# Kernel optimization log

Hardware: AMD Instinct MI355X
Metric: run time of the kernel (lower is better)

## Reference

```python
import jax, jax.numpy as jnp
import numpy as np

B, S, D, H, F, R = 4, 128, 512, 8, 2048, 8
DH = D // H
THRESH = 0.1  # hardcoded in the torch module


def _ln(x, g, b):
    m = x.mean(-1, keepdims=True)
    v = ((x - m) ** 2).mean(-1, keepdims=True)
    return (x - m) * jax.lax.rsqrt(v + 1e-5) * g + b


def setup_inputs() -> dict:
    key = jax.random.key(0)
    ks = jax.random.split(key, 12)
    w = lambda k, shape, std: jax.random.normal(k, shape, jnp.float32) * std
    s = 1.0 / np.sqrt(D)
    qk_std = 2.0 / np.sqrt(D)  # peaky attention so adjacency threshold fires
    return {
        "x": jax.random.normal(ks[0], (B, S, D), jnp.float32),
        "ln1_g": jnp.ones(D, jnp.float32), "ln1_b": jnp.zeros(D, jnp.float32),
        "wq": w(ks[1], (D, D), qk_std), "bq": jnp.zeros(D, jnp.float32),
        "wk": w(ks[2], (D, D), qk_std), "bk": jnp.zeros(D, jnp.float32),
        "wv": w(ks[3], (D, D), s), "bv": jnp.zeros(D, jnp.float32),
        "wo": w(ks[4], (D, D), s), "bo": jnp.zeros(D, jnp.float32),
        "w1": w(ks[5], (D, F), s), "b1": jnp.zeros(F, jnp.float32),
        "w2": w(ks[6], (F, D), 1.0 / np.sqrt(F)), "b2": jnp.zeros(D, jnp.float32),
        "rc_w1": w(ks[7], (2 * D, D), 1.0 / np.sqrt(2 * D)), "rc_b1": jnp.zeros(D, jnp.float32),
        "rc_w2": w(ks[8], (D, R), s), "rc_b2": jnp.zeros(R, jnp.float32),
        "kg_w": w(ks[9], (R, D, D), s),
        "s2n_w": w(ks[10], (D, D), s), "s2n_b": jnp.zeros(D, jnp.float32),
        "ln2_g": jnp.ones(D, jnp.float32), "ln2_b": jnp.zeros(D, jnp.float32),
    }


def reference(x, ln1_g, ln1_b, wq, bq, wk, bk, wv, bv, wo, bo,
              w1, b1, w2, b2, rc_w1, rc_b1, rc_w2, rc_b2,
              kg_w, s2n_w, s2n_b, ln2_g, ln2_b):
    # pre-norm attention
    xn = _ln(x, ln1_g, ln1_b)
    q = (xn @ wq + bq).reshape(B, S, H, DH)
    k = (xn @ wk + bk).reshape(B, S, H, DH)
    v = (xn @ wv + bv).reshape(B, S, H, DH)
    scores = jnp.einsum('bihd,bjhd->bhij', q, k) / np.sqrt(DH)
    attn = jax.nn.softmax(scores, axis=-1)                  # [B,H,S,S]
    ctx = jnp.einsum('bhij,bjhd->bihd', attn, v).reshape(B, S, D)
    attn_out = ctx @ wo + bo
    # FFN -> neural_understanding (no residual, as in source)
    nu = jax.nn.relu(attn_out @ w1 + b1) @ w2 + b2          # [B,S,D]
    # dynamic edge extraction, expressed as a dense mask (jit-safe)
    am = attn.mean(axis=1)                                  # [B,S,S]
    adj = (am > THRESH) & (~jnp.eye(S, dtype=bool))         # u != v
    # relation classifier on every (u,v) pair; mask selects real edges
    a_part = nu @ rc_w1[:D]                                 # concept1 half
    b_part = nu @ rc_w1[D:]                                 # concept2 half
    h = jax.nn.relu(a_part[:, :, None, :] + b_part[:, None, :, :] + rc_b1)  # [B,S,S,D]
    logits = h @ rc_w2 + rc_b2                              # [B,S,S,R]
    pred = jnp.argmax(logits, axis=-1)
    valid = adj & (pred != 0)                               # relation 0 == NONE
    oh = jax.nn.one_hot(pred, R, dtype=nu.dtype) * valid[..., None].astype(nu.dtype)
    # RGCN-style knowledge graph conv: message u -> v with per-relation weight
    transformed = jnp.einsum('bud,rde->bure', nu, kg_w)     # [B,S,R,D]
    agg = jnp.einsum('buvr,bure->bve', oh, transformed)     # [B,S,D]
    reasoned = nu + agg
    neural_result = reasoned @ s2n_w + s2n_b
    out = _ln(x + neural_result, ln2_g, ln2_b)
    return out
```

## Files before the change

### kernel.cpp

```cpp
#include <hip/hip_runtime.h>
#include <hip/hip_bf16.h>

#define B_ 4
#define S_ 128
#define D_ 512
#define H_ 8
#define DH_ 64
#define F_ 2048
#define R_ 8
#define BS_ (B_ * S_)
#define BSD_ (BS_ * D_)
#define E_ 262144

typedef __attribute__((ext_vector_type(8))) short short8;
typedef __attribute__((ext_vector_type(4))) float f32x4;
typedef __attribute__((ext_vector_type(4))) unsigned short ushort4v;

__device__ __forceinline__ void split2(float a, unsigned short& h, unsigned short& l) {
    unsigned u = __float_as_uint(a);
    unsigned hr = (u + 0x7FFFu + ((u >> 16) & 1u)) >> 16;
    h = (unsigned short)hr;
    float lo = a - __uint_as_float(hr << 16);
    unsigned u2 = __float_as_uint(lo);
    l = (unsigned short)((u2 + 0x7FFFu + ((u2 >> 16) & 1u)) >> 16);
}

struct TDesc { const float* s; unsigned short* h; unsigned short* l; int K; int N; int off; };
struct TPack { TDesc d[10]; };

__global__ void prep_kernel(TPack p, int nt, const float* __restrict__ x,
                            const float* __restrict__ g, const float* __restrict__ be,
                            unsigned short* __restrict__ xh, unsigned short* __restrict__ xl,
                            int* __restrict__ ecount) {
    __shared__ float tr[32][33];
    __shared__ float red[256];
    int bid = blockIdx.x;
    if (bid == 0 && threadIdx.x == 0) *ecount = 0;
    if (bid < nt) {
        int wi = 0;
#pragma unroll
        for (int i = 1; i < 10; ++i) if (bid >= p.d[i].off) wi = i;
        const TDesc dd = p.d[wi];
        int t = bid - dd.off;
        int ntk = dd.K / 32;
        int tk = t % ntk, tn = t / ntk;
        int k0 = tk * 32, n0 = tn * 32;
        int col = threadIdx.x & 31, rg = threadIdx.x >> 5;
#pragma unroll
        for (int i = 0; i < 4; ++i) {
            int row = rg * 4 + i;
            tr[row][col] = dd.s[(size_t)(k0 + row) * dd.N + n0 + col];
        }
        __syncthreads();
#pragma unroll
        for (int i = 0; i < 4; ++i) {
            int n = n0 + rg * 4 + i;
            int k = k0 + col;
            unsigned short h, l;
            split2(tr[col][rg * 4 + i], h, l);
            dd.h[(size_t)n * dd.K + k] = h;
            dd.l[(size_t)n * dd.K + k] = l;
        }
    } else {
        int row = bid - nt;
        int t = threadIdx.x;
        const float* xr = x + (size_t)row * D_;
        float v0 = xr[t], v1 = xr[t + 256];
        red[t] = v0 + v1;
        __syncthreads();
        for (int off = 128; off > 0; off >>= 1) { if (t < off) red[t] += red[t + off]; __syncthreads(); }
        float mean = red[0] * (1.0f / D_);
        __syncthreads();
        float d0 = v0 - mean, d1 = v1 - mean;
        red[t] = d0 * d0 + d1 * d1;
        __syncthreads();
        for (int off = 128; off > 0; off >>= 1) { if (t < off) red[t] += red[t + off]; __syncthreads(); }
        float rs = rsqrtf(red[0] * (1.0f / D_) + 1e-5f);
        float o0 = d0 * rs * g[t] + be[t];
        float o1 = d1 * rs * g[t + 256] + be[t + 256];
        unsigned short h, l;
        split2(o0, h, l); xh[(size_t)row * D_ + t] = h;       xl[(size_t)row * D_ + t] = l;
        split2(o1, h, l); xh[(size_t)row * D_ + t + 256] = h; xl[(size_t)row * D_ + t + 256] = l;
    }
}

struct GemmLds {
    unsigned short A[2][2][64][32];
    unsigned short B[2][2][64][32];
};

__device__ __forceinline__ void gload16(const unsigned short* g, unsigned short* l) {
    __builtin_amdgcn_global_load_lds(
        (const __attribute__((address_space(1))) void*)g,
        (__attribute__((address_space(3))) void*)l, 16, 0, 0);
}

__device__ __forceinline__ void mgemm_core(const unsigned short* __restrict__ Ath,
                                           const unsigned short* __restrict__ Atl,
                                           const unsigned short* __restrict__ Bth,
                                           const unsigned short* __restrict__ Btl,
                                           int K, int rowBase, int colBase,
                                           int kStart, int nsteps,
                                           f32x4 acc[2][2], GemmLds* L) {
    int tid = threadIdx.x;
    int w = tid >> 6, lane = tid & 63;
    int lm = lane & 15, quad = lane >> 4;
    int wm = (w & 1) * 32, wn = (w >> 1) * 32;
    int rS = tid >> 2;
    int cSrc = ((tid & 3) ^ (rS & 3)) * 8;
    int wb = w * 512;
    int qs = (quad ^ (lm & 3)) * 8;
    size_t aoff = (size_t)(rowBase + rS) * K + kStart + cSrc;
    size_t boff = (size_t)(colBase + rS) * K + kStart + cSrc;
    gload16(&Ath[aoff], &L->A[0][0][0][0] + wb);
    gload16(&Atl[aoff], &L->A[0][1][0][0] + wb);
    gload16(&Bth[boff], &L->B[0][0][0][0] + wb);
    gload16(&Btl[boff], &L->B[0][1][0][0] + wb);
    __syncthreads();
    for (int s = 0; s < nsteps; ++s) {
        int p = s & 1;
        if (s + 1 < nsteps) {
            int pn = p ^ 1;
            size_t ao = aoff + (size_t)(s + 1) * 32;
            size_t bo = boff + (size_t)(s + 1) * 32;
            gload16(&Ath[ao], &L->A[pn][0][0][0] + wb);
            gload16(&Atl[ao], &L->A[pn][1][0][0] + wb);
            gload16(&Bth[bo], &L->B[pn][0][0][0] + wb);
            gload16(&Btl[bo], &L->B[pn][1][0][0] + wb);
        }
        short8 ah[2], al[2], bh[2], bl[2];
#pragma unroll
        for (int t = 0; t < 2; ++t) {
            ah[t] = *(const short8*)&L->A[p][0][wm + t * 16 + lm][qs];
            al[t] = *(const short8*)&L->A[p][1][wm + t * 16 + lm][qs];
            bh[t] = *(const short8*)&L->B[p][0][wn + t * 16 + lm][qs];
            bl[t] = *(const short8*)&L->B[p][1][wn + t * 16 + lm][qs];
        }
#pragma unroll
        for (int tm = 0; tm < 2; ++tm)
#pragma unroll
            for (int tn = 0; tn < 2; ++tn) {
                acc[tm][tn] = __builtin_amdgcn_mfma_f32_16x16x32_bf16(ah[tm], bh[tn], acc[tm][tn], 0, 0, 0);
                acc[tm][tn] = __builtin_amdgcn_mfma_f32_16x16x32_bf16(ah[tm], bl[tn], acc[tm][tn], 0, 0, 0);
                acc[tm][tn] = __builtin_amdgcn_mfma_f32_16x16x32_bf16(al[tm], bh[tn], acc[tm][tn], 0, 0, 0);
            }
        __syncthreads();
    }
}

__global__ __launch_bounds__(256) void mgemm_kernel(const unsigned short* __restrict__ Ath,
                                                    const unsigned short* __restrict__ Atl,
                                                    const unsigned short* __restrict__ Bth,
                                                    const unsigned short* __restrict__ Btl,
                                                    const float* __restrict__ bias,
                                                    float* __restrict__ Cf,
                                                    unsigned short* __restrict__ Ch,
                                                    unsigned short* __restrict__ Cl,
                                                    int N, int K, int relu) {
    __shared__ GemmLds L;
    int tid = threadIdx.x;
    int w = tid >> 6, lane = tid & 63;
    int lm = lane & 15, quad = lane >> 4;
    int wm = (w & 1) * 32, wn = (w >> 1) * 32;
    int rowBase = blockIdx.y * 64, colBase = blockIdx.x * 64;
    f32x4 acc[2][2] = {};
    mgemm_core(Ath, Atl, Bth, Btl, K, rowBase, colBase, 0, K / 32, acc, &L);
#pragma unroll
    for (int tm = 0; tm < 2; ++tm)
#pragma unroll
        for (int tn = 0; tn < 2; ++tn) {
            int col = colBase + wn + tn * 16 + lm;
            float bi = bias ? bias[col] : 0.f;
#pragma unroll
            for (int r = 0; r < 4; ++r) {
                int row = rowBase + wm + tm * 16 + quad * 4 + r;
                float v = acc[tm][tn][r] + bi;
                if (relu) v = fmaxf(v, 0.f);
                size_t o = (size_t)row * N + col;
                if (Cf) Cf[o] = v;
                if (Ch) {
                    unsigned short sh, sl;
                    split2(v, sh, sl);
                    Ch[o] = sh; Cl[o] = sl;
                }
            }
        }
}

__global__ __launch_bounds__(256) void mgemm_zw_kernel(const unsigned short* __restrict__ Ath,
                                                       const unsigned short* __restrict__ Atl,
                                                       const unsigned short* __restrict__ Bth,
                                                       const unsigned short* __restrict__ Btl,
                                                       const float* __restrict__ b0,
                                                       const float* __restrict__ b1,
                                                       const float* __restrict__ b2,
                                                       float* __restrict__ Cbase,
                                                       int M, int N, int K) {
    __shared__ GemmLds L;
    int z = blockIdx.z;
    const unsigned short* bth = Bth + (size_t)z * K * N;
    const unsigned short* btl = Btl + (size_t)z * K * N;
    const float* bias = (z == 0) ? b0 : (z == 1) ? b1 : b2;
    float* C = Cbase + (size_t)z * M * N;
    int tid = threadIdx.x;
    int w = tid >> 6, lane = tid & 63;
    int lm = lane & 15, quad = lane >> 4;
    int wm = (w & 1) * 32, wn = (w >> 1) * 32;
    int rowBase = blockIdx.y * 64, colBase = blockIdx.x * 64;
    f32x4 acc[2][2] = {};
    mgemm_core(Ath, Atl, bth, btl, K, rowBase, colBase, 0, K / 32, acc, &L);
#pragma unroll
    for (int tm = 0; tm < 2; ++tm)
#pragma unroll
        for (int tn = 0; tn < 2; ++tn) {
            int col = colBase + wn + tn * 16 + lm;
            float bi = bias ? bias[col] : 0.f;
#pragma unroll
            for (int r = 0; r < 4; ++r) {
                int row = rowBase + wm + tm * 16 + quad * 4 + r;
                C[(size_t)row * N + col] = acc[tm][tn][r] + bi;
            }
        }
}

__global__ __launch_bounds__(256) void mgemm_part_kernel(const unsigned short* __restrict__ Ath,
                                                         const unsigned short* __restrict__ Atl,
                                                         const unsigned short* __restrict__ Bth,
                                                         const unsigned short* __restrict__ Btl,
                                                         float* __restrict__ Cbase,
                                                         int M, int N, int K) {
    __shared__ GemmLds L;
    int ks = gridDim.z, z = blockIdx.z;
    int kLen = K / ks, kStart = z * kLen;
    float* C = Cbase + (size_t)z * M * N;
    int tid = threadIdx.x;
    int w = tid >> 6, lane = tid & 63;
    int lm = lane & 15, quad = lane >> 4;
    int wm = (w & 1) * 32, wn = (w >> 1) * 32;
    int rowBase = blockIdx.y * 64, colBase = blockIdx.x * 64;
    f32x4 acc[2][2] = {};
    mgemm_core(Ath, Atl, Bth, Btl, K, rowBase, colBase, kStart, kLen / 32, acc, &L);
#pragma unroll
    for (int tm = 0; tm < 2; ++tm)
#pragma unroll
        for (int tn = 0; tn < 2; ++tn) {
            int col = colBase + wn + tn * 16 + lm;
#pragma unroll
            for (int r = 0; r < 4; ++r) {
                int row = rowBase + wm + tm * 16 + quad * 4 + r;
                C[(size_t)row * N + col] = acc[tm][tn][r];
            }
        }
}

__global__ void reduce4_kernel(const float* __restrict__ part, const float* __restrict__ b2,
                               float* __restrict__ nu,
                               unsigned short* __restrict__ nh, unsigned short* __restrict__ nl) {
    int base = blockIdx.x * 1024 + threadIdx.x * 4;
    f32x4 s = *(const f32x4*)&b2[base & (D_ - 1)];
#pragma unroll
    for (int z = 0; z < 4; ++z) s += *(const f32x4*)&part[(size_t)z * BSD_ + base];
    *(f32x4*)&nu[base] = s;
    ushort4v hv, lv;
#pragma unroll
    for (int i = 0; i < 4; ++i) { unsigned short h, l; split2(s[i], h, l); hv[i] = h; lv[i] = l; }
    *(ushort4v*)&nh[base] = hv;
    *(ushort4v*)&nl[base] = lv;
}

__global__ void reduce8_kernel(const float* __restrict__ part, const float* __restrict__ nu,
                               unsigned short* __restrict__ rh, unsigned short* __restrict__ rl) {
    int base = blockIdx.x * 1024 + threadIdx.x * 4;
    f32x4 s = *(const f32x4*)&nu[base];
#pragma unroll
    for (int z = 0; z < 8; ++z) s += *(const f32x4*)&part[(size_t)z * BSD_ + base];
    ushort4v hv, lv;
#pragma unroll
    for (int i = 0; i < 4; ++i) { unsigned short h, l; split2(s[i], h, l); hv[i] = h; lv[i] = l; }
    *(ushort4v*)&rh[base] = hv;
    *(ushort4v*)&rl[base] = lv;
}

__global__ __launch_bounds__(512) void attn_fused_kernel(const float* __restrict__ q,
                                                         const float* __restrict__ k,
                                                         const float* __restrict__ v,
                                                         unsigned short* __restrict__ ch,
                                                         unsigned short* __restrict__ cl,
                                                         int* __restrict__ ecount,
                                                         int* __restrict__ elist,
                                                         int* __restrict__ rel) {
    __shared__ float qsm[H_][DH_];
    __shared__ float psm[H_][S_];
    int h = threadIdx.x >> 6, lane = threadIdx.x & 63;
    int blk = blockIdx.x;
    int i = blk & (S_ - 1);
    int b = blk >> 7;
    const float* qrow = q + (size_t)(b * S_ + i) * D_ + h * DH_;
    qsm[h][lane] = qrow[lane];
    __syncthreads();
    float s0 = 0.f, s1 = 0.f;
    const float* k0p = k + (size_t)(b * S_ + lane) * D_ + h * DH_;
    const float* k1p = k0p + (size_t)64 * D_;
#pragma unroll 8
    for (int d = 0; d < DH_; ++d) {
        float qd = qsm[h][d];
        s0 += qd * k0p[d];
        s1 += qd * k1p[d];
    }
    s0 *= 0.125f; s1 *= 0.125f;
    float m = fmaxf(s0, s1);
#pragma unroll
    for (int off = 32; off > 0; off >>= 1) m = fmaxf(m, __shfl_xor(m, off));
    float e0 = __expf(s0 - m), e1 = __expf(s1 - m);
    float sum = e0 + e1;
#pragma unroll
    for (int off = 32; off > 0; off >>= 1) sum += __shfl_xor(sum, off);
    float inv = 1.f / sum;
    psm[h][lane] = e0 * inv;
    psm[h][lane + 64] = e1 * inv;
    __syncthreads();
    if (threadIdx.x < S_) {
        int j = threadIdx.x;
        rel[(size_t)blk * S_ + j] = 0;
        float s = 0.f;
#pragma unroll
        for (int hh = 0; hh < H_; ++hh) s += psm[hh][j];
        s *= (1.0f / H_);
        if (s > 0.1f && i != j) {
            int p = atomicAdd(ecount, 1);
            elist[p] = blk * S_ + j;
        }
    }
    const float* vbase = v + (size_t)b * S_ * D_ + h * DH_ + lane;
    float acc = 0.f;
    for (int j = 0; j < S_; ++j) acc += psm[h][j] * vbase[(size_t)j * D_];
    unsigned short sh, sl;
    split2(acc, sh, sl);
    size_t o = (size_t)(b * S_ + i) * D_ + h * DH_ + lane;
    ch[o] = sh; cl[o] = sl;
}

__global__ __launch_bounds__(256) void edge_kernel(const float* __restrict__ a_part,
                                                   const float* __restrict__ b_part,
                                                   const float* __restrict__ rc_b1,
                                                   const float* __restrict__ rc_w2,
                                                   const float* __restrict__ rc_b2,
                                                   const int* __restrict__ elist,
                                                   const int* __restrict__ ecount,
                                                   int* __restrict__ rel) {
    int w = threadIdx.x >> 6, lane = threadIdx.x & 63;
    int n = *ecount;
    for (int e = blockIdx.x * 4 + w; e < n; e += gridDim.x * 4) {
        int idx = elist[e];
        int vv = idx & (S_ - 1);
        int bu = idx >> 7;
        int u = bu & (S_ - 1);
        int b = bu >> 7;
        const float* ap = a_part + (size_t)(b * S_ + u) * D_;
        const float* bp = b_part + (size_t)(b * S_ + vv) * D_;
        float lp[R_];
#pragma unroll
        for (int r = 0; r < R_; ++r) lp[r] = 0.f;
#pragma unroll
        for (int jj = 0; jj < D_ / 64; ++jj) {
            int d = lane + jj * 64;
            float hv = fmaxf(ap[d] + bp[d] + rc_b1[d], 0.f);
#pragma unroll
            for (int r = 0; r < R_; ++r) lp[r] += hv * rc_w2[d * R_ + r];
        }
#pragma unroll
        for (int r = 0; r < R_; ++r) {
#pragma unroll
            for (int off = 32; off > 0; off >>= 1) lp[r] += __shfl_down(lp[r], off);
        }
        if (lane == 0) {
            float best = lp[0] + rc_b2[0];
            int bi = 0;
#pragma unroll
            for (int r = 1; r < R_; ++r) {
                float L = lp[r] + rc_b2[r];
                if (L > best) { best = L; bi = r; }
            }
            rel[idx] = bi;
        }
    }
}

__global__ __launch_bounds__(128) void mbuild_kernel(const float* __restrict__ nu,
                                                     const int* __restrict__ rel,
                                                     unsigned short* __restrict__ Mh,
                                                     unsigned short* __restrict__ Ml) {
    __shared__ float acc[R_ * D_];
    __shared__ int rl[S_];
    int blk = blockIdx.x;
    int vv = blk & (S_ - 1);
    int b = blk >> 7;
    int t = threadIdx.x;
    for (int i = t; i < R_ * D_; i += 128) acc[i] = 0.f;
    rl[t] = rel[((size_t)b * S_ + t) * S_ + vv];
    __syncthreads();
    for (int u = 0; u < S_; ++u) {
        int r = rl[u];
        if (r > 0) {
            const float* nurow = nu + (size_t)(b * S_ + u) * D_;
            float* arow = acc + r * D_;
#pragma unroll
            for (int jj = 0; jj < D_ / 128; ++jj) arow[t + jj * 128] += nurow[t + jj * 128];
        }
    }
    __syncthreads();
    unsigned short* Hrow = Mh + (size_t)blk * (R_ * D_);
    unsigned short* Lrow = Ml + (size_t)blk * (R_ * D_);
    for (int i = t; i < R_ * D_; i += 128) {
        unsigned short sh, sl;
        split2(acc[i], sh, sl);
        Hrow[i] = sh; Lrow[i] = sl;
    }
}

__global__ void ln2_kernel(const float* __restrict__ x, const float* __restrict__ y,
                           const float* __restrict__ g, const float* __restrict__ be,
                           float* __restrict__ out) {
    int row = blockIdx.x;
    int t = threadIdx.x;
    __shared__ float red[256];
    float v0 = x[row * D_ + t]       + y[row * D_ + t];
    float v1 = x[row * D_ + t + 256] + y[row * D_ + t + 256];
    red[t] = v0 + v1;
    __syncthreads();
    for (int off = 128; off > 0; off >>= 1) {
        if (t < off) red[t] += red[t + off];
        __syncthreads();
    }
    float mean = red[0] * (1.0f / D_);
    __syncthreads();
    float d0 = v0 - mean, d1 = v1 - mean;
    red[t] = d0 * d0 + d1 * d1;
    __syncthreads();
    for (int off = 128; off > 0; off >>= 1) {
        if (t < off) red[t] += red[t + off];
        __syncthreads();
    }
    float rs = rsqrtf(red[0] * (1.0f / D_) + 1e-5f);
    out[row * D_ + t]       = d0 * rs * g[t]       + be[t];
    out[row * D_ + t + 256] = d1 * rs * g[t + 256] + be[t + 256];
}

extern "C" void kernel_launch(void* const* d_in, const int* in_sizes, int n_in,
                              void* d_out, int out_size, void* d_ws, size_t ws_size,
                              hipStream_t stream) {
    const float* x     = (const float*)d_in[0];
    const float* ln1_g = (const float*)d_in[1];
    const float* ln1_b = (const float*)d_in[2];
    const float* wq    = (const float*)d_in[3];
    const float* bq    = (const float*)d_in[4];
    const float* wk    = (const float*)d_in[5];
    const float* bk    = (const float*)d_in[6];
    const float* wv    = (const float*)d_in[7];
    const float* bv    = (const float*)d_in[8];
    const float* wo    = (const float*)d_in[9];
    const float* bo    = (const float*)d_in[10];
    const float* w1    = (const float*)d_in[11];
    const float* b1    = (const float*)d_in[12];
    const float* w2    = (const float*)d_in[13];
    const float* b2    = (const float*)d_in[14];
    const float* rc_w1 = (const float*)d_in[15];
    const float* rc_b1 = (const float*)d_in[16];
    const float* rc_w2 = (const float*)d_in[17];
    const float* rc_b2 = (const float*)d_in[18];
    const float* kg_w  = (const float*)d_in[19];
    const float* s2n_w = (const float*)d_in[20];
    const float* s2n_b = (const float*)d_in[21];
    const float* ln2_g = (const float*)d_in[22];
    const float* ln2_b = (const float*)d_in[23];
    float* out = (float*)d_out;

    const int BS  = BS_;
    const int BSD = BSD_;

    unsigned short* wt = (unsigned short*)d_ws;
    unsigned short* qkv_h = wt;
    unsigned short* qkv_l = wt + 3 * E_;
    unsigned short* wo_h  = wt + 6 * E_;
    unsigned short* wo_l  = wt + 7 * E_;
    unsigned short* w1_h  = wt + 8 * E_;
    unsigned short* w1_l  = wt + 12 * E_;
    unsigned short* w2_h  = wt + 16 * E_;
    unsigned short* w2_l  = wt + 20 * E_;
    unsigned short* rc_h  = wt + 24 * E_;
    unsigned short* rc_l  = wt + 26 * E_;
    unsigned short* kg_h  = wt + 28 * E_;
    unsigned short* kg_l  = wt + 36 * E_;
    unsigned short* s2_h  = wt + 44 * E_;
    unsigned short* s2_l  = wt + 45 * E_;

    unsigned short* xn_h  = wt + 46 * E_;
    unsigned short* xn_l  = xn_h + BSD;
    unsigned short* ctx_h = xn_l + BSD;
    unsigned short* ctx_l = ctx_h + BSD;
    unsigned short* ao_h  = ctx_l + BSD;
    unsigned short* ao_l  = ao_h + BSD;
    unsigned short* hid_h = ao_l + BSD;
    unsigned short* hid_l = hid_h + (size_t)BS * F_;
    unsigned short* nu_h  = hid_l + (size_t)BS * F_;
    unsigned short* nu_l  = nu_h + BSD;
    unsigned short* mb_h  = nu_l + BSD;
    unsigned short* mb_l  = mb_h + (size_t)BS * R_ * D_;
    unsigned short* rs_h  = mb_l + (size_t)BS * R_ * D_;
    unsigned short* rs_l  = rs_h + BSD;

    float* fbase  = (float*)(rs_l + BSD);
    float* q      = fbase;
    float* v_     = q + 2 * BSD;
    float* apart  = q + 3 * BSD;
    float* nu     = apart + 2 * BSD;
    float* y      = nu + BSD;
    float* part4  = y + BSD;
    float* part8  = part4 + 4 * BSD;

    int* rel    = (int*)(part8 + 8 * BSD);
    int* ecount = rel + B_ * S_ * S_;
    int* elist  = ecount + 64;

    TPack tp;
    int off = 0;
    auto setd = [&](int i, const float* s, unsigned short* h, unsigned short* l, int K, int N) {
        tp.d[i] = TDesc{s, h, l, K, N, off};
        off += (K / 32) * (N / 32);
    };
    setd(0, wq, qkv_h,          qkv_l,          D_, D_);
    setd(1, wk, qkv_h + E_,     qkv_l + E_,     D_, D_);
    setd(2, wv, qkv_h + 2 * E_, qkv_l + 2 * E_, D_, D_);
    setd(3, wo, wo_h, wo_l, D_, D_);
    setd(4, w1, w1_h, w1_l, D_, F_);
    setd(5, w2, w2_h, w2_l, F_, D_);
    setd(6, rc_w1,            rc_h,      rc_l,      D_, D_);
    setd(7, rc_w1 + D_ * D_,  rc_h + E_, rc_l + E_, D_, D_);
    setd(8, kg_w, kg_h, kg_l, R_ * D_, D_);
    setd(9, s2n_w, s2_h, s2_l, D_, D_);
    hipLaunchKernelGGL(prep_kernel, dim3(off + BS), dim3(256), 0, stream, tp, off,
                       x, ln1_g, ln1_b, xn_h, xn_l, ecount);

    hipLaunchKernelGGL(mgemm_zw_kernel, dim3(D_ / 64, BS / 64, 3), dim3(256), 0, stream,
                       xn_h, xn_l, qkv_h, qkv_l, bq, bk, bv, q, BS, D_, D_);
    hipLaunchKernelGGL(attn_fused_kernel, dim3(BS), dim3(512), 0, stream,
                       q, q + BSD, v_, ctx_h, ctx_l, ecount, elist, rel);
    hipLaunchKernelGGL(mgemm_kernel, dim3(D_ / 64, BS / 64), dim3(256), 0, stream,
                       ctx_h, ctx_l, wo_h, wo_l, bo, (float*)nullptr, ao_h, ao_l, D_, D_, 0);
    hipLaunchKernelGGL(mgemm_kernel, dim3(F_ / 64, BS / 64), dim3(256), 0, stream,
                       ao_h, ao_l, w1_h, w1_l, b1, (float*)nullptr, hid_h, hid_l, F_, D_, 1);
    hipLaunchKernelGGL(mgemm_part_kernel, dim3(D_ / 64, BS / 64, 4), dim3(256), 0, stream,
                       hid_h, hid_l, w2_h, w2_l, part4, BS, D_, F_);
    hipLaunchKernelGGL(reduce4_kernel, dim3(BSD / 1024), dim3(256), 0, stream,
                       part4, b2, nu, nu_h, nu_l);
    hipLaunchKernelGGL(mgemm_zw_kernel, dim3(D_ / 64, BS / 64, 2), dim3(256), 0, stream,
                       nu_h, nu_l, rc_h, rc_l, (const float*)nullptr, (const float*)nullptr,
                       (const float*)nullptr, apart, BS, D_, D_);
    hipLaunchKernelGGL(edge_kernel, dim3(256), dim3(256), 0, stream,
                       apart, apart + BSD, rc_b1, rc_w2, rc_b2, elist, ecount, rel);
    hipLaunchKernelGGL(mbuild_kernel, dim3(BS), dim3(128), 0, stream, nu, rel, mb_h, mb_l);
    hipLaunchKernelGGL(mgemm_part_kernel, dim3(D_ / 64, BS / 64, 8), dim3(256), 0, stream,
                       mb_h, mb_l, kg_h, kg_l, part8, BS, D_, R_ * D_);
    hipLaunchKernelGGL(reduce8_kernel, dim3(BSD / 1024), dim3(256), 0, stream,
                       part8, nu, rs_h, rs_l);
    hipLaunchKernelGGL(mgemm_kernel, dim3(D_ / 64, BS / 64), dim3(256), 0, stream,
                       rs_h, rs_l, s2_h, s2_l, s2n_b, y, (unsigned short*)nullptr,
                       (unsigned short*)nullptr, D_, D_, 0);
    hipLaunchKernelGGL(ln2_kernel, dim3(BS), dim3(256), 0, stream, x, y, ln2_g, ln2_b, out);
}
```

Before: 245.5 us.

## Widen GEMM K-tile, restructure attention per head-block, fuse adjacency into Wo GEMM

The shared GEMM core now stages a 64-wide K tile per step instead of 32, with a new XOR swizzle. This halves the number of barriers and loop iterations. Attention is reorganised so each block handles 16 query rows of one head and caches K in LDS. It writes the probabilities to a buffer, and the adjacency/edge-list pass moves into extra blocks of a combined Wo GEMM launch. The edge kernel also transposes rc_w2 into LDS. The cost is double the GEMM LDS footprint, which may lower occupancy, plus an extra 8 MB round trip for the attention probabilities.

```diff
diff --git a/kernel.cpp b/kernel.cpp
--- a/kernel.cpp
+++ b/kernel.cpp
@@ -85,8 +85,8 @@
 }
 
 struct GemmLds {
-    unsigned short A[2][2][64][32];
-    unsigned short B[2][2][64][32];
+    unsigned short A[2][2][64][64];
+    unsigned short B[2][2][64][64];
 };
 
 __device__ __forceinline__ void gload16(const unsigned short* g, unsigned short* l) {
@@ -106,65 +106,63 @@
     int w = tid >> 6, lane = tid & 63;
     int lm = lane & 15, quad = lane >> 4;
     int wm = (w & 1) * 32, wn = (w >> 1) * 32;
-    int rS = tid >> 2;
-    int cSrc = ((tid & 3) ^ (rS & 3)) * 8;
+    int r0 = w * 8 + (lane >> 3);
+    int lc = ((lane & 7) ^ (lane >> 3)) * 8;
     int wb = w * 512;
-    int qs = (quad ^ (lm & 3)) * 8;
-    size_t aoff = (size_t)(rowBase + rS) * K + kStart + cSrc;
-    size_t boff = (size_t)(colBase + rS) * K + kStart + cSrc;
-    gload16(&Ath[aoff], &L->A[0][0][0][0] + wb);
-    gload16(&Atl[aoff], &L->A[0][1][0][0] + wb);
-    gload16(&Bth[boff], &L->B[0][0][0][0] + wb);
-    gload16(&Btl[boff], &L->B[0][1][0][0] + wb);
+    size_t a0 = (size_t)(rowBase + r0) * K + kStart + lc;
+    size_t a1 = (size_t)(rowBase + r0 + 32) * K + kStart + lc;
+    size_t b0 = (size_t)(colBase + r0) * K + kStart + lc;
+    size_t b1 = (size_t)(colBase + r0 + 32) * K + kStart + lc;
+    unsigned short* AB = &L->A[0][0][0][0];
+    unsigned short* BB = &L->B[0][0][0][0];
+    auto stage = [&](int p, size_t koff) {
+        gload16(&Ath[a0 + koff], AB + p * 8192 + wb);
+        gload16(&Ath[a1 + koff], AB + p * 8192 + 2048 + wb);
+        gload16(&Atl[a0 + koff], AB + p * 8192 + 4096 + wb);
+        gload16(&Atl[a1 + koff], AB + p * 8192 + 6144 + wb);
+        gload16(&Bth[b0 + koff], BB + p * 8192 + wb);
+        gload16(&Bth[b1 + koff], BB + p * 8192 + 2048 + wb);
+        gload16(&Btl[b0 + koff], BB + p * 8192 + 4096 + wb);
+        gload16(&Btl[b1 + koff], BB + p * 8192 + 6144 + wb);
+    };
+    stage(0, 0);
     __syncthreads();
     for (int s = 0; s < nsteps; ++s) {
         int p = s & 1;
-        if (s + 1 < nsteps) {
-            int pn = p ^ 1;
-            size_t ao = aoff + (size_t)(s + 1) * 32;
-            size_t bo = boff + (size_t)(s + 1) * 32;
-            gload16(&Ath[ao], &L->A[pn][0][0][0] + wb);
-            gload16(&Atl[ao], &L->A[pn][1][0][0] + wb);
-            gload16(&Bth[bo], &L->B[pn][0][0][0] + wb);
-            gload16(&Btl[bo], &L->B[pn][1][0][0] + wb);
-        }
-        short8 ah[2], al[2], bh[2], bl[2];
-#pragma unroll
-        for (int t = 0; t < 2; ++t) {
-            ah[t] = *(const short8*)&L->A[p][0][wm + t * 16 + lm][qs];
-            al[t] = *(const short8*)&L->A[p][1][wm + t * 16 + lm][qs];
-            bh[t] = *(const short8*)&L->B[p][0][wn + t * 16 + lm][qs];
-            bl[t] = *(const short8*)&L->B[p][1][wn + t * 16 + lm][qs];
-        }
-#pragma unroll
-        for (int tm = 0; tm < 2; ++tm)
-#pragma unroll
-            for (int tn = 0; tn < 2; ++tn) {
-                acc[tm][tn] = __builtin_amdgcn_mfma_f32_16x16x32_bf16(ah[tm], bh[tn], acc[tm][tn], 0, 0, 0);
-                acc[tm][tn] = __builtin_amdgcn_mfma_f32_16x16x32_bf16(ah[tm], bl[tn], acc[tm][tn], 0, 0, 0);
-                acc[tm][tn] = __builtin_amdgcn_mfma_f32_16x16x32_bf16(al[tm], bh[tn], acc[tm][tn], 0, 0, 0);
+        if (s + 1 < nsteps) stage(p ^ 1, (size_t)(s + 1) * 64);
+#pragma unroll
+        for (int sub = 0; sub < 2; ++sub) {
+            short8 ah[2], al[2], bh[2], bl[2];
+            int pc = ((sub * 4 + quad) ^ (lm & 7)) * 8;
+#pragma unroll
+            for (int t = 0; t < 2; ++t) {
+                int ra = (wm + t * 16 + lm) * 64 + pc;
+                int rb = (wn + t * 16 + lm) * 64 + pc;
+                ah[t] = *(const short8*)(AB + p * 8192 + ra);
+                al[t] = *(const short8*)(AB + p * 8192 + 4096 + ra);
+                bh[t] = *(const short8*)(BB + p * 8192 + rb);
+                bl[t] = *(const short8*)(BB + p * 8192 + 4096 + rb);
             }
-        __syncthreads();
-    }
-}
-
-__global__ __launch_bounds__(256) void mgemm_kernel(const unsigned short* __restrict__ Ath,
-                                                    const unsigned short* __restrict__ Atl,
-                                                    const unsigned short* __restrict__ Bth,
-                                                    const unsigned short* __restrict__ Btl,
-                                                    const float* __restrict__ bias,
-                                                    float* __restrict__ Cf,
-                                                    unsigned short* __restrict__ Ch,
-                                                    unsigned short* __restrict__ Cl,
-                                                    int N, int K, int relu) {
-    __shared__ GemmLds L;
+#pragma unroll
+            for (int tm = 0; tm < 2; ++tm)
+#pragma unroll
+                for (int tn = 0; tn < 2; ++tn) {
+                    acc[tm][tn] = __builtin_amdgcn_mfma_f32_16x16x32_bf16(ah[tm], bh[tn], acc[tm][tn], 0, 0, 0);
+                    acc[tm][tn] = __builtin_amdgcn_mfma_f32_16x16x32_bf16(ah[tm], bl[tn], acc[tm][tn], 0, 0, 0);
+                    acc[tm][tn] = __builtin_amdgcn_mfma_f32_16x16x32_bf16(al[tm], bh[tn], acc[tm][tn], 0, 0, 0);
+                }
+        }
+        __syncthreads();
+    }
+}
+
+__device__ __forceinline__ void gemm_epilogue(f32x4 acc[2][2], const float* bias,
+                                              float* Cf, unsigned short* Ch, unsigned short* Cl,
+                                              int N, int relu, int rowBase, int colBase) {
     int tid = threadIdx.x;
     int w = tid >> 6, lane = tid & 63;
     int lm = lane & 15, quad = lane >> 4;
     int wm = (w & 1) * 32, wn = (w >> 1) * 32;
-    int rowBase = blockIdx.y * 64, colBase = blockIdx.x * 64;
-    f32x4 acc[2][2] = {};
-    mgemm_core(Ath, Atl, Bth, Btl, K, rowBase, colBase, 0, K / 32, acc, &L);
 #pragma unroll
     for (int tm = 0; tm < 2; ++tm)
 #pragma unroll
@@ -185,6 +183,22 @@
                 }
             }
         }
+}
+
+__global__ __launch_bounds__(256) void mgemm_kernel(const unsigned short* __restrict__ Ath,
+                                                    const unsigned short* __restrict__ Atl,
+                                                    const unsigned short* __restrict__ Bth,
+                                                    const unsigned short* __restrict__ Btl,
+                                                    const float* __restrict__ bias,
+                                                    float* __restrict__ Cf,
+                                                    unsigned short* __restrict__ Ch,
+                                                    unsigned short* __restrict__ Cl,
+                                                    int N, int K, int relu) {
+    __shared__ GemmLds L;
+    int rowBase = blockIdx.y * 64, colBase = blockIdx.x * 64;
+    f32x4 acc[2][2] = {};
+    mgemm_core(Ath, Atl, Bth, Btl, K, rowBase, colBase, 0, K / 64, acc, &L);
+    gemm_epilogue(acc, bias, Cf, Ch, Cl, N, relu, rowBase, colBase);
 }
 
 __global__ __launch_bounds__(256) void mgemm_zw_kernel(const unsigned short* __restrict__ Ath,
@@ -202,25 +216,10 @@
     const unsigned short* btl = Btl + (size_t)z * K * N;
     const float* bias = (z == 0) ? b0 : (z == 1) ? b1 : b2;
     float* C = Cbase + (size_t)z * M * N;
-    int tid = threadIdx.x;
-    int w = tid >> 6, lane = tid & 63;
-    int lm = lane & 15, quad = lane >> 4;
-    int wm = (w & 1) * 32, wn = (w >> 1) * 32;
     int rowBase = blockIdx.y * 64, colBase = blockIdx.x * 64;
     f32x4 acc[2][2] = {};
-    mgemm_core(Ath, Atl, bth, btl, K, rowBase, colBase, 0, K / 32, acc, &L);
-#pragma unroll
-    for (int tm = 0; tm < 2; ++tm)
-#pragma unroll
-        for (int tn = 0; tn < 2; ++tn) {
-            int col = colBase + wn + tn * 16 + lm;
-            float bi = bias ? bias[col] : 0.f;
-#pragma unroll
-            for (int r = 0; r < 4; ++r) {
-                int row = rowBase + wm + tm * 16 + quad * 4 + r;
-                C[(size_t)row * N + col] = acc[tm][tn][r] + bi;
-            }
-        }
+    mgemm_core(Ath, Atl, bth, btl, K, rowBase, colBase, 0, K / 64, acc, &L);
+    gemm_epilogue(acc, bias, C, nullptr, nullptr, N, 0, rowBase, colBase);
 }
 
 __global__ __launch_bounds__(256) void mgemm_part_kernel(const unsigned short* __restrict__ Ath,
@@ -233,24 +232,46 @@
     int ks = gridDim.z, z = blockIdx.z;
     int kLen = K / ks, kStart = z * kLen;
     float* C = Cbase + (size_t)z * M * N;
-    int tid = threadIdx.x;
-    int w = tid >> 6, lane = tid & 63;
-    int lm = lane & 15, quad = lane >> 4;
-    int wm = (w & 1) * 32, wn = (w >> 1) * 32;
     int rowBase = blockIdx.y * 64, colBase = blockIdx.x * 64;
     f32x4 acc[2][2] = {};
-    mgemm_core(Ath, Atl, Bth, Btl, K, rowBase, colBase, kStart, kLen / 32, acc, &L);
-#pragma unroll
-    for (int tm = 0; tm < 2; ++tm)
-#pragma unroll
-        for (int tn = 0; tn < 2; ++tn) {
-            int col = colBase + wn + tn * 16 + lm;
-#pragma unroll
-            for (int r = 0; r < 4; ++r) {
-                int row = rowBase + wm + tm * 16 + quad * 4 + r;
-                C[(size_t)row * N + col] = acc[tm][tn][r];
-            }
-        }
+    mgemm_core(Ath, Atl, Bth, Btl, K, rowBase, colBase, kStart, kLen / 64, acc, &L);
+    gemm_epilogue(acc, nullptr, C, nullptr, nullptr, N, 0, rowBase, colBase);
+}
+
+__global__ __launch_bounds__(256) void wo_adj_kernel(const unsigned short* __restrict__ Ath,
+                                                     const unsigned short* __restrict__ Atl,
+                                                     const unsigned short* __restrict__ Bth,
+                                                     const unsigned short* __restrict__ Btl,
+                                                     const float* __restrict__ bias,
+                                                     unsigned short* __restrict__ Ch,
+                                                     unsigned short* __restrict__ Cl,
+                                                     const float* __restrict__ attnP,
+                                                     int* __restrict__ ecount,
+                                                     int* __restrict__ elist,
+                                                     int* __restrict__ rel) {
+    __shared__ GemmLds L;
+    int bid = blockIdx.x;
+    if (bid < 64) {
+        int rowBase = (bid >> 3) * 64, colBase = (bid & 7) * 64;
+        f32x4 acc[2][2] = {};
+        mgemm_core(Ath, Atl, Bth, Btl, D_, rowBase, colBase, 0, D_ / 64, acc, &L);
+        gemm_epilogue(acc, bias, nullptr, Ch, Cl, D_, 0, rowBase, colBase);
+    } else {
+        int idx = (bid - 64) * 256 + threadIdx.x;
+        int j = idx & (S_ - 1);
+        int bi = idx >> 7;
+        int i = bi & (S_ - 1);
+        int b = bi >> 7;
+        float s = 0.f;
+#pragma unroll
+        for (int h = 0; h < H_; ++h) s += attnP[(((size_t)(b * H_ + h)) * S_ + i) * S_ + j];
+        s *= (1.0f / H_);
+        rel[idx] = 0;
+        if (s > 0.1f && i != j) {
+            int p = atomicAdd(ecount, 1);
+            elist[p] = idx;
+        }
+    }
 }
 
 __global__ void reduce4_kernel(const float* __restrict__ part, const float* __restrict__ b2,
@@ -281,63 +302,62 @@
     *(ushort4v*)&rl[base] = lv;
 }
 
-__global__ __launch_bounds__(512) void attn_fused_kernel(const float* __restrict__ q,
-                                                         const float* __restrict__ k,
-                                                         const float* __restrict__ v,
-                                                         unsigned short* __restrict__ ch,
-                                                         unsigned short* __restrict__ cl,
-                                                         int* __restrict__ ecount,
-                                                         int* __restrict__ elist,
-                                                         int* __restrict__ rel) {
-    __shared__ float qsm[H_][DH_];
-    __shared__ float psm[H_][S_];
-    int h = threadIdx.x >> 6, lane = threadIdx.x & 63;
+__global__ __launch_bounds__(512) void attn_kernel2(const float* __restrict__ q,
+                                                    const float* __restrict__ k,
+                                                    const float* __restrict__ v,
+                                                    float* __restrict__ attnP,
+                                                    unsigned short* __restrict__ ch,
+                                                    unsigned short* __restrict__ cl) {
+    __shared__ float ksm[S_][DH_ + 3];
+    __shared__ float qsm[16][DH_];
+    __shared__ float psm[16][S_];
+    int tid = threadIdx.x;
+    int w = tid >> 6, lane = tid & 63;
     int blk = blockIdx.x;
-    int i = blk & (S_ - 1);
-    int b = blk >> 7;
-    const float* qrow = q + (size_t)(b * S_ + i) * D_ + h * DH_;
-    qsm[h][lane] = qrow[lane];
-    __syncthreads();
-    float s0 = 0.f, s1 = 0.f;
-    const float* k0p = k + (size_t)(b * S_ + lane) * D_ + h * DH_;
-    const float* k1p = k0p + (size_t)64 * D_;
+    int ig = blk & 7;
+    int bh = blk >> 3;
+    int h = bh & (H_ - 1);
+    int b = bh >> 3;
+    int i0 = ig * 16;
+    const float* kb = k + (size_t)b * S_ * D_ + h * DH_;
+    for (int j = w; j < S_; j += 8) ksm[j][lane] = kb[(size_t)j * D_ + lane];
+    for (int il = w; il < 16; il += 8)
+        qsm[il][lane] = q[(size_t)(b * S_ + i0 + il) * D_ + h * DH_ + lane];
+    __syncthreads();
+    const float* vb = v + (size_t)b * S_ * D_ + h * DH_ + lane;
+#pragma unroll
+    for (int c = 0; c < 2; ++c) {
+        int il = w + c * 8;
+        int i = i0 + il;
+        float s0 = 0.f, s1 = 0.f;
 #pragma unroll 8
-    for (int d = 0; d < DH_; ++d) {
-        float qd = qsm[h][d];
-        s0 += qd * k0p[d];
-        s1 += qd * k1p[d];
-    }
-    s0 *= 0.125f; s1 *= 0.125f;
-    float m = fmaxf(s0, s1);
-#pragma unroll
-    for (int off = 32; off > 0; off >>= 1) m = fmaxf(m, __shfl_xor(m, off));
-    float e0 = __expf(s0 - m), e1 = __expf(s1 - m);
-    float sum = e0 + e1;
-#pragma unroll
-    for (int off = 32; off > 0; off >>= 1) sum += __shfl_xor(sum, off);
-    float inv = 1.f / sum;
-    psm[h][lane] = e0 * inv;
-    psm[h][lane + 64] = e1 * inv;
-    __syncthreads();
-    if (threadIdx.x < S_) {
-        int j = threadIdx.x;
-        rel[(size_t)blk * S_ + j] = 0;
-        float s = 0.f;
-#pragma unroll
-        for (int hh = 0; hh < H_; ++hh) s += psm[hh][j];
-        s *= (1.0f / H_);
-        if (s > 0.1f && i != j) {
-            int p = atomicAdd(ecount, 1);
-            elist[p] = blk * S_ + j;
-        }
-    }
-    const float* vbase = v + (size_t)b * S_ * D_ + h * DH_ + lane;
-    float acc = 0.f;
-    for (int j = 0; j < S_; ++j) acc += psm[h][j] * vbase[(size_t)j * D_];
-    unsigned short sh, sl;
-    split2(acc, sh, sl);
-    size_t o = (size_t)(b * S_ + i) * D_ + h * DH_ + lane;
-    ch[o] = sh; cl[o] = sl;
+        for (int d = 0; d < DH_; ++d) {
+            float qd = qsm[il][d];
+            s0 += qd * ksm[lane][d];
+            s1 += qd * ksm[lane + 64][d];
+        }
+        s0 *= 0.125f; s1 *= 0.125f;
+        float m = fmaxf(s0, s1);
+#pragma unroll
+        for (int off = 32; off > 0; off >>= 1) m = fmaxf(m, __shfl_xor(m, off));
+        float e0 = __expf(s0 - m), e1 = __expf(s1 - m);
+        float sum = e0 + e1;
+#pragma unroll
+        for (int off = 32; off > 0; off >>= 1) sum += __shfl_xor(sum, off);
+        float inv = 1.f / sum;
+        float p0 = e0 * inv, p1 = e1 * inv;
+        float* arow = attnP + ((size_t)(b * H_ + h) * S_ + i) * S_;
+        arow[lane] = p0;
+        arow[lane + 64] = p1;
+        psm[il][lane] = p0;
+        psm[il][lane + 64] = p1;
+        float acc = 0.f;
+        for (int j = 0; j < S_; ++j) acc += psm[il][j] * vb[(size_t)j * D_];
+        unsigned short sh, sl;
+        split2(acc, sh, sl);
+        size_t o = (size_t)(b * S_ + i) * D_ + h * DH_ + lane;
+        ch[o] = sh; cl[o] = sl;
+    }
 }
 
 __global__ __launch_bounds__(256) void edge_kernel(const float* __restrict__ a_part,
@@ -348,6 +368,10 @@
                                                    const int* __restrict__ elist,
                                                    const int* __restrict__ ecount,
                                                    int* __restrict__ rel) {
+    __shared__ float w2t[R_][D_];
+    for (int idx = threadIdx.x; idx < R_ * D_; idx += 256)
+        w2t[idx & 7][idx >> 3] = rc_w2[idx];
+    __syncthreads();
     int w = threadIdx.x >> 6, lane = threadIdx.x & 63;
     int n = *ecount;
     for (int e = blockIdx.x * 4 + w; e < n; e += gridDim.x * 4) {
@@ -366,7 +390,7 @@
             int d = lane + jj * 64;
             float hv = fmaxf(ap[d] + bp[d] + rc_b1[d], 0.f);
 #pragma unroll
-            for (int r = 0; r < R_; ++r) lp[r] += hv * rc_w2[d * R_ + r];
+            for (int r = 0; r < R_; ++r) lp[r] += hv * w2t[r][d];
         }
 #pragma unroll
         for (int r = 0; r < R_; ++r) {
@@ -517,8 +541,9 @@
     float* y      = nu + BSD;
     float* part4  = y + BSD;
     float* part8  = part4 + 4 * BSD;
-
-    int* rel    = (int*)(part8 + 8 * BSD);
+    float* attnP  = part8 + 8 * BSD;
+
+    int* rel    = (int*)(attnP + 2097152);
     int* ecount = rel + B_ * S_ * S_;
     int* elist  = ecount + 64;
 
@@ -543,10 +568,10 @@
 
     hipLaunchKernelGGL(mgemm_zw_kernel, dim3(D_ / 64, BS / 64, 3), dim3(256), 0, stream,
                        xn_h, xn_l, qkv_h, qkv_l, bq, bk, bv, q, BS, D_, D_);
-    hipLaunchKernelGGL(attn_fused_kernel, dim3(BS), dim3(512), 0, stream,
-                       q, q + BSD, v_, ctx_h, ctx_l, ecount, elist, rel);
-    hipLaunchKernelGGL(mgemm_kernel, dim3(D_ / 64, BS / 64), dim3(256), 0, stream,
-                       ctx_h, ctx_l, wo_h, wo_l, bo, (float*)nullptr, ao_h, ao_l, D_, D_, 0);
+    hipLaunchKernelGGL(attn_kernel2, dim3(B_ * H_ * 8), dim3(512), 0, stream,
+                       q, q + BSD, v_, attnP, ctx_h, ctx_l);
+    hipLaunchKernelGGL(wo_adj_kernel, dim3(64 + 256), dim3(256), 0, stream,
+                       ctx_h, ctx_l, wo_h, wo_l, bo, ao_h, ao_l, attnP, ecount, elist, rel);
     hipLaunchKernelGGL(mgemm_kernel, dim3(F_ / 64, BS / 64), dim3(256), 0, stream,
                        ao_h, ao_l, w1_h, w1_l, b1, (float*)nullptr, hid_h, hid_l, F_, D_, 1);
     hipLaunchKernelGGL(mgemm_part_kernel, dim3(D_ / 64, BS / 64, 4), dim3(256), 0, stream,
```

Measured after the change: 228.1 us. 7.1% less time.
